# Optimization experiments

Hardware: AMD Instinct MI355X
Metric: run time of the kernel (lower is better)

## Reference

```python
import jax, jax.numpy as jnp
import numpy as np

NUM_CODES = 1024
CODE_DIM = 256
EMA_DECAY = 0.99
COMMITMENT = 0.25
EPS = 1e-6


def setup_inputs() -> dict:
    key = jax.random.key(0)
    k1, k2 = jax.random.split(key)
    z = jax.random.normal(k1, (64, 512, CODE_DIM), dtype=jnp.float32)
    embedding = jax.random.normal(k2, (NUM_CODES, CODE_DIM), dtype=jnp.float32)
    cluster_size = jnp.zeros((NUM_CODES,), dtype=jnp.float32)
    embedding_avg = embedding.copy()
    return {"z": z, "embedding": embedding, "cluster_size": cluster_size,
            "embedding_avg": embedding_avg}


def reference(z, embedding, cluster_size, embedding_avg):
    K, D = embedding.shape
    flat = z.reshape(-1, D)                                  # [N, D]
    dist = (jnp.sum(flat * flat, axis=1, keepdims=True)
            - 2.0 * (flat @ embedding.T)
            + jnp.sum(embedding * embedding, axis=1))
    indices = jnp.argmin(dist, axis=1)                       # [N]
    z_q = embedding[indices].reshape(z.shape)

    # EMA codebook update (training branch, no-grad in original)
    counts = jax.ops.segment_sum(jnp.ones_like(indices, dtype=flat.dtype),
                                 indices, num_segments=K)    # one-hot col sums
    embed_sum = jax.ops.segment_sum(flat, indices, num_segments=K)  # [K, D]
    new_cluster_size = cluster_size * EMA_DECAY + (1.0 - EMA_DECAY) * counts
    new_embedding_avg = embedding_avg * EMA_DECAY + (1.0 - EMA_DECAY) * embed_sum
    n = jnp.sum(new_cluster_size)
    cs = (new_cluster_size + EPS) / (n + K * EPS)
    new_embedding = new_embedding_avg / cs[:, None]

    loss = COMMITMENT * jnp.mean((jax.lax.stop_gradient(z_q) - z) ** 2)
    z_q_st = z + jax.lax.stop_gradient(z_q - z)
    return (z_q_st, loss, indices, new_cluster_size, new_embedding_avg,
            new_embedding)
```

## Files before the change

kernel.cpp:

```cpp
#include <hip/hip_runtime.h>

#define N_ROWS   32768
#define KCODES   1024
#define DDIM     256
#define RPB      64
#define NBLK     512

#define O_ZQ     0
#define O_LOSS   8388608
#define O_IDX    8388609
#define O_NCS    8421377
#define O_NEA    8422401
#define O_NEMB   8684545

#define W_ESUM   0
#define W_CNT    262144
#define W_DONE   263168
#define W_ENORM  264192
#define W_LOSSP  265216
#define W_N      265728
#define W_IDX    265792
#define W_SORT   298560
#define W_RANK   331328

typedef _Float16 half_t;
typedef __attribute__((ext_vector_type(8))) _Float16 half8;
typedef __attribute__((ext_vector_type(4))) float floatx4;

__global__ __launch_bounds__(256)
void k_prep2(const float* __restrict__ emb, float* __restrict__ enorm,
             half_t* __restrict__ Bp, float* __restrict__ zero_ws) {
    __shared__ half_t hi[16 * 256];
    __shared__ half_t lo[16 * 256];
    __shared__ float  ssum[256];
    const int ct  = blockIdx.x;
    const int tid = threadIdx.x;
    const int c16 = tid >> 4;
    const int dp  = tid & 15;

    {
        float4 z4 = {0.f, 0.f, 0.f, 0.f};
        float4* wsf4 = (float4*)zero_ws;
        int t = ct * 256 + tid;
        #pragma unroll
        for (int i = 0; i < 4; ++i) wsf4[t + i * 16384] = z4;
        if (t < 512) wsf4[65536 + t] = z4;
    }

    float ss = 0.f;
    #pragma unroll
    for (int i = 0; i < 4; ++i) {
        float4 v = *(const float4*)(emb + (size_t)(ct * 16 + c16) * DDIM + dp * 16 + i * 4);
        ss += v.x * v.x + v.y * v.y + v.z * v.z + v.w * v.w;
        #pragma unroll
        for (int q = 0; q < 4; ++q) {
            float f = (&v.x)[q];
            half_t h = (half_t)f;
            hi[c16 * 256 + dp * 16 + i * 4 + q] = h;
            lo[c16 * 256 + dp * 16 + i * 4 + q] = (half_t)(f - (float)h);
        }
    }
    ssum[tid] = ss;
    __syncthreads();
    if (tid < 16) {
        float s = 0.f;
        #pragma unroll
        for (int i = 0; i < 16; ++i) s += ssum[tid * 16 + i];
        enorm[ct * 16 + tid] = s;
    }

    const int g16 = ((ct >> 4) << 2) | ((ct >> 2) & 3);
    const int ns  = ct & 3;
    #pragma unroll
    for (int i = 0; i < 4; ++i) {
        int f    = tid + i * 256;
        int ks   = f >> 6;
        int lane = f & 63;
        int cc   = lane & 15;
        int seg  = ks >> 3;
        int ko   = (ks & 7) * 32 + (lane >> 4) * 8;
        const half_t* src = (seg == 1) ? lo : hi;
        half8 v = *(const half8*)(src + cc * 256 + ko);
        *(half8*)(Bp + (((size_t)(g16 * 16 + ks) * 4 + ns) * 64 + lane) * 8) = v;
    }
}

__global__ __launch_bounds__(512)
void k_argmin(const float* __restrict__ z, const half_t* __restrict__ Bp,
              const float* __restrict__ enorm, const float* __restrict__ embf,
              int* __restrict__ out_idx, float* __restrict__ out_idx_f,
              float* __restrict__ out_zq, float* __restrict__ lossp,
              int* __restrict__ counts_i, int* __restrict__ rank_ws) {
    __shared__ __align__(16) half_t As[RPB * 512];

    const int tid  = threadIdx.x;
    const int w    = tid >> 6;
    const int lane = tid & 63;
    const int tx   = lane & 15;
    const int quad = lane >> 4;
    const int rbase = blockIdx.x * RPB;

    {
        const int arow = w * 8 + (lane >> 3);
        const int sw   = arow & 7;
        #pragma unroll
        for (int it = 0; it < 4; ++it) {
            int g = it * 8 + (lane & 7);
            const float* zp = z + (size_t)(rbase + arow) * DDIM + g * 8;
            float4 v0 = *(const float4*)zp;
            float4 v1 = *(const float4*)(zp + 4);
            half8 hi, lo;
            hi[0] = (half_t)v0.x; lo[0] = (half_t)(v0.x - (float)hi[0]);
            hi[1] = (half_t)v0.y; lo[1] = (half_t)(v0.y - (float)hi[1]);
            hi[2] = (half_t)v0.z; lo[2] = (half_t)(v0.z - (float)hi[2]);
            hi[3] = (half_t)v0.w; lo[3] = (half_t)(v0.w - (float)hi[3]);
            hi[4] = (half_t)v1.x; lo[4] = (half_t)(v1.x - (float)hi[4]);
            hi[5] = (half_t)v1.y; lo[5] = (half_t)(v1.y - (float)hi[5]);
            hi[6] = (half_t)v1.z; lo[6] = (half_t)(v1.z - (float)hi[6]);
            hi[7] = (half_t)v1.w; lo[7] = (half_t)(v1.w - (float)hi[7]);
            *(half8*)(&As[arow * 512 + ((g ^ sw)) * 8])        = hi;
            *(half8*)(&As[arow * 512 + (((32 + g) ^ sw)) * 8]) = lo;
        }
    }
    __syncthreads();

    floatx4 zero4 = {0.f, 0.f, 0.f, 0.f};
    float bd[4][4];
    int   bi[4][4];
    #pragma unroll
    for (int mt = 0; mt < 4; ++mt)
        #pragma unroll
        for (int r = 0; r < 4; ++r) { bd[mt][r] = 3.402823466e38f; bi[mt][r] = 0; }

    for (int g = 0; g < 4; ++g) {
        const int slot = 2 * w + (g >> 1);
        const int ns0  = (g & 1) * 2;
        const int cb   = (slot >> 2) * 256 + (slot & 3) * 64 + ns0 * 16;
        const half_t* Bg = Bp + (size_t)slot * 32768 + ns0 * 512 + (size_t)lane * 8;

        floatx4 acc[4][2];
        #pragma unroll
        for (int mt = 0; mt < 4; ++mt)
            #pragma unroll
            for (int ns = 0; ns < 2; ++ns) acc[mt][ns] = zero4;

        half8 B0[2], B1[2];
        #define LOADB(PK, BUF)                                                 \
            { const half_t* bp_ = Bg + (PK) * 2048;                            \
              BUF[0] = *(const half8*)(bp_);                                   \
              BUF[1] = *(const half8*)(bp_ + 512); }
        #define LDA(K8)                                                        \
            _Pragma("unroll")                                                  \
            for (int mt = 0; mt < 4; ++mt) {                                   \
                int row = mt * 16 + tx;                                        \
                a[mt] = *(half8*)(&As[row * 512 + (((K8) + quad) ^ (row & 7)) * 8]); \
            }
        #define MFMA_BLK(BUF)                                                  \
            _Pragma("unroll")                                                  \
            for (int mt = 0; mt < 4; ++mt)                                     \
                _Pragma("unroll")                                              \
                for (int ns = 0; ns < 2; ++ns)                                 \
                    acc[mt][ns] = __builtin_amdgcn_mfma_f32_16x16x32_f16(      \
                        a[mt], BUF[ns], acc[mt][ns], 0, 0, 0);

        LOADB(0, B0);
        LOADB(1, B1);

        #pragma unroll 2
        for (int s = 0; s < 8; ++s) {
            half8 a[4];
            LDA(s * 4)
            if (s & 1) { MFMA_BLK(B1) } else { MFMA_BLK(B0) }
            LDA(32 + s * 4)
            if (s & 1) { MFMA_BLK(B1) LOADB(s + 2, B1); }
            else       { MFMA_BLK(B0) LOADB(s + 2, B0); }
        }
        #pragma unroll 2
        for (int s = 8; s < 16; ++s) {
            half8 a[4];
            LDA((s - 8) * 4)
            if (s & 1) { MFMA_BLK(B1) if (s + 2 < 16) LOADB(s + 2, B1); }
            else       { MFMA_BLK(B0) if (s + 2 < 16) LOADB(s + 2, B0); }
        }
        #undef LOADB
        #undef LDA
        #undef MFMA_BLK

        #pragma unroll
        for (int ns = 0; ns < 2; ++ns) {
            float en = enorm[cb + ns * 16 + tx];
            int   cc = cb + ns * 16 + tx;
            #pragma unroll
            for (int mt = 0; mt < 4; ++mt)
                #pragma unroll
                for (int r = 0; r < 4; ++r) {
                    float d = fmaf(-2.f, acc[mt][ns][r], en);
                    if (d < bd[mt][r]) { bd[mt][r] = d; bi[mt][r] = cc; }
                }
        }
    }

    #pragma unroll
    for (int mt = 0; mt < 4; ++mt)
        #pragma unroll
        for (int r = 0; r < 4; ++r) {
            float d = bd[mt][r];
            int   b = bi[mt][r];
            #pragma unroll
            for (int off = 8; off > 0; off >>= 1) {
                float od = __shfl_xor(d, off);
                int   ob = __shfl_xor(b, off);
                if (od < d || (od == d && ob < b)) { d = od; b = ob; }
            }
            bd[mt][r] = d; bi[mt][r] = b;
        }

    __syncthreads();
    float* sd   = (float*)As;
    int*   si   = ((int*)As) + 512;
    int*   sidx = ((int*)As) + 1024;
    if (tx == 0) {
        #pragma unroll
        for (int mt = 0; mt < 4; ++mt)
            #pragma unroll
            for (int r = 0; r < 4; ++r) {
                int row = mt * 16 + quad * 4 + r;
                sd[row * 8 + w] = bd[mt][r];
                si[row * 8 + w] = bi[mt][r];
            }
    }
    __syncthreads();
    if (tid < RPB) {
        int row = tid;
        float d = sd[row * 8];
        int   b = si[row * 8];
        #pragma unroll
        for (int ww = 1; ww < 8; ++ww) {
            float od = sd[row * 8 + ww];
            int   ob = si[row * 8 + ww];
            if (od < d || (od == d && ob < b)) { d = od; b = ob; }
        }
        sidx[row] = b;
        out_idx[rbase + row]   = b;
        out_idx_f[rbase + row] = (float)b;
        int rk = atomicAdd(&counts_i[b], 1);
        rank_ws[rbase + row] = rk;
    }
    __syncthreads();

    float l = 0.f;
    #pragma unroll
    for (int u = 0; u < 8; ++u) {
        int gi  = tid + u * 512;
        int row = gi >> 6;
        int c4  = gi & 63;
        int k   = sidx[row];
        float4 zv = *(const float4*)(z    + (size_t)(rbase + row) * DDIM + c4 * 4);
        float4 ev = *(const float4*)(embf + (size_t)k * DDIM + c4 * 4);
        float dx = ev.x - zv.x, dy = ev.y - zv.y, dz = ev.z - zv.z, dw = ev.w - zv.w;
        float4 o = { zv.x + dx, zv.y + dy, zv.z + dz, zv.w + dw };
        *(float4*)(out_zq + (size_t)(rbase + row) * DDIM + c4 * 4) = o;
        l += dx * dx + dy * dy + dz * dz + dw * dw;
    }
    #pragma unroll
    for (int off = 32; off > 0; off >>= 1) l += __shfl_down(l, off);
    __shared__ float ls[8];
    if (lane == 0) ls[w] = l;
    __syncthreads();
    if (tid == 0) {
        float s = 0.f;
        #pragma unroll
        for (int i = 0; i < 8; ++i) s += ls[i];
        lossp[blockIdx.x] = s;
    }
}

__global__ __launch_bounds__(256)
void k_scatter(const float* __restrict__ cs_in, const int* __restrict__ counts_i,
               const float* __restrict__ lossp, const int* __restrict__ idx,
               const int* __restrict__ rank_ws, const float* __restrict__ ea,
               int* __restrict__ rows_sorted,
               float* __restrict__ out_ncs, float* __restrict__ n_ws,
               float* __restrict__ loss_out,
               float* __restrict__ out_nea, float* __restrict__ out_nemb) {
    const int tid = threadIdx.x;
    const int bid = blockIdx.x;
    const int w    = tid >> 6;
    const int lane = tid & 63;
    __shared__ int ps[256];
    __shared__ int base_s[1024];
    __shared__ float sv[4], sl[4];

    int c[4]; int pt = 0;
    #pragma unroll
    for (int i = 0; i < 4; ++i) { c[i] = counts_i[tid * 4 + i]; pt += c[i]; }
    ps[tid] = pt;
    __syncthreads();
    for (int s = 1; s < 256; s <<= 1) {
        int v = (tid >= s) ? ps[tid - s] : 0;
        __syncthreads();
        ps[tid] += v;
        __syncthreads();
    }
    int o = ps[tid] - pt;
    float pn = 0.f;
    #pragma unroll
    for (int i = 0; i < 4; ++i) {
        base_s[tid * 4 + i] = o;
        o += c[i];
        float nc = cs_in[tid * 4 + i] * 0.99f + 0.01f * (float)c[i];
        pn += nc;
        if (bid == 0) out_ncs[tid * 4 + i] = nc;
    }
    float pl = (bid == 0) ? (lossp[tid] + lossp[tid + 256]) : 0.f;
    #pragma unroll
    for (int off = 32; off > 0; off >>= 1) {
        pn += __shfl_down(pn, off);
        pl += __shfl_down(pl, off);
    }
    if (lane == 0) { sv[w] = pn; sl[w] = pl; }
    __syncthreads();
    const float nval = sv[0] + sv[1] + sv[2] + sv[3];
    if (bid == 0 && tid == 0) {
        n_ws[0]     = nval;
        loss_out[0] = 0.25f * ((sl[0] + sl[1] + sl[2] + sl[3]) / 8388608.0f);
    }
    {
        int r = bid * 256 + tid;
        int k = idx[r];
        rows_sorted[base_s[k] + rank_ws[r]] = r;
    }
    #pragma unroll
    for (int pass = 0; pass < 2; ++pass) {
        int k = bid * 8 + pass * 4 + (tid >> 6);
        if (counts_i[k] == 0) {
            int l2 = tid & 63;
            size_t off = (size_t)k * DDIM + l2 * 4;
            float4 av = *(const float4*)(ea + off);
            float4 nea = { av.x * 0.99f, av.y * 0.99f, av.z * 0.99f, av.w * 0.99f };
            *(float4*)(out_nea + off) = nea;
            float ncv = cs_in[k] * 0.99f;
            float csv = (ncv + 1e-6f) / (nval + 0.001024f);
            float4 nemb = { nea.x / csv, nea.y / csv, nea.z / csv, nea.w / csv };
            *(float4*)(out_nemb + off) = nemb;
        }
    }
}

__global__ __launch_bounds__(256)
void k_esum3(const float* __restrict__ z, const int* __restrict__ rows_sorted,
             const int* __restrict__ idx, const int* __restrict__ counts_i,
             const float* __restrict__ cs_in, const float* __restrict__ n_ws,
             const float* __restrict__ ea, float* __restrict__ esum,
             int* __restrict__ done,
             float* __restrict__ out_nea, float* __restrict__ out_nemb) {
    const int tid  = threadIdx.x;
    const int w    = tid >> 6;
    const int lane = tid & 63;
    const int base = (blockIdx.x * 4 + w) * 32;
    const float nval = n_ws[0];

    int r = rows_sorted[base + (lane & 31)];
    int c = idx[r];
    float4 acc = {0.f, 0.f, 0.f, 0.f};
    int rlen = 0;
    #pragma unroll 4
    for (int j = 0; j < 32; ++j) {
        int rj = __shfl(r, j);
        int cj = __shfl(c, j);
        float4 zv = *(const float4*)(z + (size_t)rj * DDIM + lane * 4);
        acc.x += zv.x; acc.y += zv.y; acc.z += zv.z; acc.w += zv.w;
        rlen++;
        int cn = (j < 31) ? __shfl(c, j + 1) : -1;
        if (cn != cj) {
            float* p = esum + (size_t)cj * DDIM + lane * 4;
            atomicAdd(p + 0, acc.x);
            atomicAdd(p + 1, acc.y);
            atomicAdd(p + 2, acc.z);
            atomicAdd(p + 3, acc.w);
            asm volatile("s_waitcnt vmcnt(0)" ::: "memory");
            int last = 0;
            if (lane == 0) {
                int old = atomicAdd(&done[cj], rlen);
                last = (old + rlen == counts_i[cj]) ? 1 : 0;
            }
            last = __shfl(last, 0);
            if (last) {
                float* q = esum + (size_t)cj * DDIM + lane * 4;
                float4 ev;
                ev.x = atomicAdd(q + 0, 0.f);
                ev.y = atomicAdd(q + 1, 0.f);
                ev.z = atomicAdd(q + 2, 0.f);
                ev.w = atomicAdd(q + 3, 0.f);
                size_t off = (size_t)cj * DDIM + lane * 4;
                float4 av = *(const float4*)(ea + off);
                float4 nea = { av.x * 0.99f + 0.01f * ev.x,
                               av.y * 0.99f + 0.01f * ev.y,
                               av.z * 0.99f + 0.01f * ev.z,
                               av.w * 0.99f + 0.01f * ev.w };
                *(float4*)(out_nea + off) = nea;
                float ncv = cs_in[cj] * 0.99f + 0.01f * (float)counts_i[cj];
                float csv = (ncv + 1e-6f) / (nval + 0.001024f);
                float4 nemb = { nea.x / csv, nea.y / csv, nea.z / csv, nea.w / csv };
                *(float4*)(out_nemb + off) = nemb;
            }
            acc.x = 0.f; acc.y = 0.f; acc.z = 0.f; acc.w = 0.f;
            rlen = 0;
        }
    }
}

extern "C" void kernel_launch(void* const* d_in, const int* in_sizes, int n_in,
                              void* d_out, int out_size, void* d_ws, size_t ws_size,
                              hipStream_t stream) {
    const float* z   = (const float*)d_in[0];
    const float* emb = (const float*)d_in[1];
    const float* cs  = (const float*)d_in[2];
    const float* ea  = (const float*)d_in[3];
    float* out = (float*)d_out;
    float* ws  = (float*)d_ws;

    float* esum    = ws + W_ESUM;
    int*   cnts    = (int*)(ws + W_CNT);
    int*   done    = (int*)(ws + W_DONE);
    float* enorm   = ws + W_ENORM;
    float* lossp   = ws + W_LOSSP;
    float* wn      = ws + W_N;
    int*   widx    = (int*)(ws + W_IDX);
    int*   rsorted = (int*)(ws + W_SORT);
    int*   rankw   = (int*)(ws + W_RANK);

    half_t* Bp = (half_t*)(out + O_NEA + 3);

    k_prep2   <<<64, 256, 0, stream>>>(emb, enorm, Bp, ws);
    k_argmin  <<<NBLK, 512, 0, stream>>>(z, Bp, enorm, emb,
                                         widx, out + O_IDX, out + O_ZQ, lossp,
                                         cnts, rankw);
    k_scatter <<<128, 256, 0, stream>>>(cs, cnts, lossp, widx, rankw, ea,
                                        rsorted, out + O_NCS, wn, out + O_LOSS,
                                        out + O_NEA, out + O_NEMB);
    k_esum3   <<<256, 256, 0, stream>>>(z, rsorted, widx, cnts, cs, wn, ea,
                                        esum, done, out + O_NEA, out + O_NEMB);
}
```

Before: 184.3 us.

## Retile argmin MFMA as 2x4 warp grid with double-buffered A fragments

Each of the 8 waves now covers 32 rows by a contiguous 256-code quarter, instead of all 64 rows by a 128-code slice. The per-wave MFMA tile becomes 2x4 rather than 4x2, which halves the LDS A-fragment reads per MFMA and doubles the global B fragment loads per wave. A fragments are software-pipelined across two register sets so LDS reads overlap the MFMAs, and s_setprio brackets the MFMA blocks. The cross-wave argmin reduction shrinks from 8 to 4 candidates per row. Costs include more B global traffic and a different register footprint.

New measurement: 191.8 us. +4.1%, slower.

```diff
diff --git a/kernel.cpp b/kernel.cpp
--- a/kernel.cpp
+++ b/kernel.cpp
@@ -98,6 +98,8 @@
     const int lane = tid & 63;
     const int tx   = lane & 15;
     const int quad = lane >> 4;
+    const int rh   = w >> 2;
+    const int cq   = w & 3;
     const int rbase = blockIdx.x * RPB;
 
     {
@@ -125,73 +127,80 @@
     __syncthreads();
 
     floatx4 zero4 = {0.f, 0.f, 0.f, 0.f};
-    float bd[4][4];
-    int   bi[4][4];
-    #pragma unroll
-    for (int mt = 0; mt < 4; ++mt)
+    float bd[2][4];
+    int   bi[2][4];
+    #pragma unroll
+    for (int mt = 0; mt < 2; ++mt)
         #pragma unroll
         for (int r = 0; r < 4; ++r) { bd[mt][r] = 3.402823466e38f; bi[mt][r] = 0; }
 
-    for (int g = 0; g < 4; ++g) {
-        const int slot = 2 * w + (g >> 1);
-        const int ns0  = (g & 1) * 2;
-        const int cb   = (slot >> 2) * 256 + (slot & 3) * 64 + ns0 * 16;
-        const half_t* Bg = Bp + (size_t)slot * 32768 + ns0 * 512 + (size_t)lane * 8;
-
-        floatx4 acc[4][2];
-        #pragma unroll
-        for (int mt = 0; mt < 4; ++mt)
+    for (int g4 = 0; g4 < 4; ++g4) {
+        const int cb = cq * 256 + g4 * 64;
+        const half_t* Bg = Bp + (size_t)(cq * 4 + g4) * 32768 + (size_t)lane * 8;
+
+        floatx4 acc[2][4];
+        #pragma unroll
+        for (int mt = 0; mt < 2; ++mt)
             #pragma unroll
-            for (int ns = 0; ns < 2; ++ns) acc[mt][ns] = zero4;
-
-        half8 B0[2], B1[2];
+            for (int ns = 0; ns < 4; ++ns) acc[mt][ns] = zero4;
+
+        half8 B0[4], B1[4];
+        half8 a0[2], a1[2];
         #define LOADB(PK, BUF)                                                 \
             { const half_t* bp_ = Bg + (PK) * 2048;                            \
-              BUF[0] = *(const half8*)(bp_);                                   \
-              BUF[1] = *(const half8*)(bp_ + 512); }
-        #define LDA(K8)                                                        \
+              _Pragma("unroll")                                                \
+              for (int ns = 0; ns < 4; ++ns)                                   \
+                  BUF[ns] = *(const half8*)(bp_ + ns * 512); }
+        #define LDA(AF, K8)                                                    \
             _Pragma("unroll")                                                  \
-            for (int mt = 0; mt < 4; ++mt) {                                   \
-                int row = mt * 16 + tx;                                        \
-                a[mt] = *(half8*)(&As[row * 512 + (((K8) + quad) ^ (row & 7)) * 8]); \
-            }
-        #define MFMA_BLK(BUF)                                                  \
+            for (int mt = 0; mt < 2; ++mt) {                                   \
+                int row = rh * 32 + mt * 16 + tx;                              \
+                AF[mt] = *(half8*)(&As[row * 512 + (((K8) + quad) ^ (row & 7)) * 8]); \
+            }
+        #define MFMA_BLK(AF, BUF)                                              \
+            __builtin_amdgcn_s_setprio(1);                                     \
             _Pragma("unroll")                                                  \
-            for (int mt = 0; mt < 4; ++mt)                                     \
+            for (int mt = 0; mt < 2; ++mt)                                     \
                 _Pragma("unroll")                                              \
-                for (int ns = 0; ns < 2; ++ns)                                 \
+                for (int ns = 0; ns < 4; ++ns)                                 \
                     acc[mt][ns] = __builtin_amdgcn_mfma_f32_16x16x32_f16(      \
-                        a[mt], BUF[ns], acc[mt][ns], 0, 0, 0);
+                        AF[mt], BUF[ns], acc[mt][ns], 0, 0, 0);                \
+            __builtin_amdgcn_s_setprio(0);
 
         LOADB(0, B0);
         LOADB(1, B1);
+        LDA(a0, 0)
 
         #pragma unroll 2
         for (int s = 0; s < 8; ++s) {
-            half8 a[4];
-            LDA(s * 4)
-            if (s & 1) { MFMA_BLK(B1) } else { MFMA_BLK(B0) }
-            LDA(32 + s * 4)
-            if (s & 1) { MFMA_BLK(B1) LOADB(s + 2, B1); }
-            else       { MFMA_BLK(B0) LOADB(s + 2, B0); }
+            LDA(a1, 32 + s * 4)
+            if (s & 1) { MFMA_BLK(a0, B1) } else { MFMA_BLK(a0, B0) }
+            LDA(a0, ((s + 1) & 7) * 4)
+            if (s & 1) { MFMA_BLK(a1, B1) LOADB(s + 2, B1); }
+            else       { MFMA_BLK(a1, B0) LOADB(s + 2, B0); }
         }
         #pragma unroll 2
         for (int s = 8; s < 16; ++s) {
-            half8 a[4];
-            LDA((s - 8) * 4)
-            if (s & 1) { MFMA_BLK(B1) if (s + 2 < 16) LOADB(s + 2, B1); }
-            else       { MFMA_BLK(B0) if (s + 2 < 16) LOADB(s + 2, B0); }
+            if (s & 1) {
+                if (s < 15) { LDA(a0, (s - 7) * 4) }
+                MFMA_BLK(a1, B1)
+                if (s + 2 < 16) LOADB(s + 2, B1);
+            } else {
+                LDA(a1, (s - 7) * 4)
+                MFMA_BLK(a0, B0)
+                if (s + 2 < 16) LOADB(s + 2, B0);
+            }
         }
         #undef LOADB
         #undef LDA
         #undef MFMA_BLK
 
         #pragma unroll
-        for (int ns = 0; ns < 2; ++ns) {
+        for (int ns = 0; ns < 4; ++ns) {
             float en = enorm[cb + ns * 16 + tx];
             int   cc = cb + ns * 16 + tx;
             #pragma unroll
-            for (int mt = 0; mt < 4; ++mt)
+            for (int mt = 0; mt < 2; ++mt)
                 #pragma unroll
                 for (int r = 0; r < 4; ++r) {
                     float d = fmaf(-2.f, acc[mt][ns][r], en);
@@ -201,7 +210,7 @@
     }
 
     #pragma unroll
-    for (int mt = 0; mt < 4; ++mt)
+    for (int mt = 0; mt < 2; ++mt)
         #pragma unroll
         for (int r = 0; r < 4; ++r) {
             float d = bd[mt][r];
@@ -217,27 +226,27 @@
 
     __syncthreads();
     float* sd   = (float*)As;
-    int*   si   = ((int*)As) + 512;
-    int*   sidx = ((int*)As) + 1024;
+    int*   si   = ((int*)As) + 256;
+    int*   sidx = ((int*)As) + 512;
     if (tx == 0) {
         #pragma unroll
-        for (int mt = 0; mt < 4; ++mt)
+        for (int mt = 0; mt < 2; ++mt)
             #pragma unroll
             for (int r = 0; r < 4; ++r) {
-                int row = mt * 16 + quad * 4 + r;
-                sd[row * 8 + w] = bd[mt][r];
-                si[row * 8 + w] = bi[mt][r];
+                int row = rh * 32 + mt * 16 + quad * 4 + r;
+                sd[row * 4 + cq] = bd[mt][r];
+                si[row * 4 + cq] = bi[mt][r];
             }
     }
     __syncthreads();
     if (tid < RPB) {
         int row = tid;
-        float d = sd[row * 8];
-        int   b = si[row * 8];
-        #pragma unroll
-        for (int ww = 1; ww < 8; ++ww) {
-            float od = sd[row * 8 + ww];
-            int   ob = si[row * 8 + ww];
+        float d = sd[row * 4];
+        int   b = si[row * 4];
+        #pragma unroll
+        for (int ww = 1; ww < 4; ++ww) {
+            float od = sd[row * 4 + ww];
+            int   ob = si[row * 4 + ww];
             if (od < d || (od == d && ob < b)) { d = od; b = ob; }
         }
         sidx[row] = b;
```
